# Optimization experiments

Hardware: AMD Instinct MI355X
Metric: run time of the kernel (lower is better)

## Reference

```python
import jax, jax.numpy as jnp
import numpy as np

N = 50000      # nodes
E = 400000     # edges
IN = 128       # in_channels
HID = 64       # hidden_channels (per head)
H = 4          # heads
OUT = 10       # classes
G = 64         # graphs in batch


def setup_inputs() -> dict:
    key = jax.random.key(0)
    ks = jax.random.split(key, 32)
    s = 0.05
    inp = {
        "x": jax.random.normal(ks[0], (N, IN), dtype=jnp.float32),
        "edge_index": jax.random.randint(ks[1], (2, E), 0, N, dtype=jnp.int32),
        "batch": jnp.sort(jax.random.randint(ks[2], (N,), 0, G, dtype=jnp.int32)),
    }
    # TransformerConv layer 1 params (in=IN -> heads*HID)
    d1 = H * HID
    inp["Wq1"] = jax.random.normal(ks[3], (IN, d1)) * s
    inp["bq1"] = jnp.zeros((d1,), jnp.float32)
    inp["Wk1"] = jax.random.normal(ks[4], (IN, d1)) * s
    inp["bk1"] = jnp.zeros((d1,), jnp.float32)
    inp["Wv1"] = jax.random.normal(ks[5], (IN, d1)) * s
    inp["bv1"] = jnp.zeros((d1,), jnp.float32)
    inp["Ws1"] = jax.random.normal(ks[6], (IN, d1)) * s   # root/skip weight
    inp["bs1"] = jnp.zeros((d1,), jnp.float32)
    # TransformerConv layer 2 params (in=H*HID -> heads*HID)
    inp["Wq2"] = jax.random.normal(ks[7], (d1, d1)) * s
    inp["bq2"] = jnp.zeros((d1,), jnp.float32)
    inp["Wk2"] = jax.random.normal(ks[8], (d1, d1)) * s
    inp["bk2"] = jnp.zeros((d1,), jnp.float32)
    inp["Wv2"] = jax.random.normal(ks[9], (d1, d1)) * s
    inp["bv2"] = jnp.zeros((d1,), jnp.float32)
    inp["Ws2"] = jax.random.normal(ks[10], (d1, d1)) * s
    inp["bs2"] = jnp.zeros((d1,), jnp.float32)
    # final classifier
    inp["Wl"] = jax.random.normal(ks[11], (d1, OUT)) * s
    inp["bl"] = jnp.zeros((OUT,), jnp.float32)
    return inp


def transformer_conv(x, src, dst, Wq, bq, Wk, bk, Wv, bv, Ws, bs):
    """PyG TransformerConv (concat=True, root_weight=True, beta=None, eval mode).
    src = edge_index[0] (source j), dst = edge_index[1] (target i).
    """
    n = x.shape[0]
    q = (x @ Wq + bq).reshape(n, H, HID)
    k = (x @ Wk + bk).reshape(n, H, HID)
    v = (x @ Wv + bv).reshape(n, H, HID)
    # per-edge attention logits [E, H]
    alpha = jnp.einsum('ehc,ehc->eh', q[dst], k[src]) / np.sqrt(HID).astype(np.float32)
    # scatter-softmax over incoming edges of each target node
    amax = jax.ops.segment_max(alpha, dst, num_segments=n)           # [N, H], -inf for isolated
    ex = jnp.exp(alpha - amax[dst])                                   # [E, H]
    denom = jax.ops.segment_sum(ex, dst, num_segments=n) + 1e-16      # [N, H]
    w = ex / denom[dst]                                               # normalized alpha [E, H]
    # scatter-sum aggregation of weighted values
    out = jax.ops.segment_sum(w[:, :, None] * v[src], dst, num_segments=n)  # [N, H, HID]
    out = out.reshape(n, H * HID)
    return out + (x @ Ws + bs)  # root/skip connection


def reference(x, edge_index, batch,
              Wq1, bq1, Wk1, bk1, Wv1, bv1, Ws1, bs1,
              Wq2, bq2, Wk2, bk2, Wv2, bv2, Ws2, bs2,
              Wl, bl):
    src, dst = edge_index[0], edge_index[1]
    h = jax.nn.elu(transformer_conv(x, src, dst, Wq1, bq1, Wk1, bk1, Wv1, bv1, Ws1, bs1))
    h = jax.nn.elu(transformer_conv(h, src, dst, Wq2, bq2, Wk2, bk2, Wv2, bv2, Ws2, bs2))
    # global mean pool per graph
    sums = jax.ops.segment_sum(h, batch, num_segments=G)              # [G, H*HID]
    cnt = jax.ops.segment_sum(jnp.ones((h.shape[0],), h.dtype), batch, num_segments=G)
    pooled = sums / jnp.maximum(cnt, 1.0)[:, None]
    logits = pooled @ Wl + bl
    return jax.nn.log_softmax(logits, axis=-1)
```

## Files before the change

kernel.cpp:

```cpp
#include <hip/hip_runtime.h>
#include <math.h>

constexpr int NN   = 50000;
constexpr int NE   = 400000;
constexpr int INC  = 128;
constexpr int NH   = 4;
constexpr int D1   = 256;
constexpr int D4   = 1024;
constexpr int NOUT = 10;
constexpr int NG   = 64;
constexpr int NB_SCAN = (NN + 255) / 256;


typedef __attribute__((ext_vector_type(8))) short bf16x8;
typedef __attribute__((ext_vector_type(4))) float f32x4;
typedef __attribute__((ext_vector_type(2))) float f32x2;

__device__ __forceinline__ short f2b(float f) {
  union { float f; unsigned int i; } v; v.f = f;
  unsigned int x = v.i;
  return (short)((x + 0x7FFFu + ((x >> 16) & 1u)) >> 16);
}
__device__ __forceinline__ float b2f(short u) {
  union { unsigned int i; float f; } v; v.i = ((unsigned int)(unsigned short)u) << 16;
  return v.f;
}
__device__ __forceinline__ float4 ld4b(const short* p) {
  short4 u = *(const short4*)p;
  return make_float4(b2f(u.x), b2f(u.y), b2f(u.z), b2f(u.w));
}
__device__ __forceinline__ void unpack8(const int4 v, float* f) {
  union { unsigned int u; float x; } a;
  a.u = (unsigned int)v.x << 16;         f[0] = a.x;
  a.u = (unsigned int)v.x & 0xffff0000u; f[1] = a.x;
  a.u = (unsigned int)v.y << 16;         f[2] = a.x;
  a.u = (unsigned int)v.y & 0xffff0000u; f[3] = a.x;
  a.u = (unsigned int)v.z << 16;         f[4] = a.x;
  a.u = (unsigned int)v.z & 0xffff0000u; f[5] = a.x;
  a.u = (unsigned int)v.w << 16;         f[6] = a.x;
  a.u = (unsigned int)v.w & 0xffff0000u; f[7] = a.x;
}
__device__ __forceinline__ int pk_fp8x4(float a, float b, float c, float d) {
  int v = __builtin_amdgcn_cvt_pk_fp8_f32(a, b, 0, false);
  v = __builtin_amdgcn_cvt_pk_fp8_f32(c, d, v, true);
  return v;
}

__device__ __forceinline__ void gld_lds16(const short* g, short* l) {
  __builtin_amdgcn_global_load_lds(
      (const __attribute__((address_space(1))) unsigned int*)g,
      (__attribute__((address_space(3))) unsigned int*)l, 16, 0, 0);
}

constexpr int CVT_XB  = (NN * INC / 4 + 255) / 256;
constexpr int CVT_W1B = (4 * D1 * INC + 255) / 256;
constexpr int CVT_W2B = (4 * D1 * D1 + 255) / 256;
constexpr int CVT_BB  = 8;
constexpr int CVT_DB  = (NN + 255) / 256;
constexpr int CVT_SB  = (NG * D1 + 255) / 256;

__device__ __forceinline__ void wt_one(const float* Wq, const float* Wk,
    const float* Wv, const float* Ws, short* Wt, int kbits, int i) {
  int K = 1 << kbits;
  int seg = i >> (kbits + 8);
  int idx = i & ((D1 << kbits) - 1);
  int n = idx >> kbits, k = idx & (K - 1);
  const float* W = (seg == 0) ? Wq : (seg == 1) ? Wk : (seg == 2) ? Wv : Ws;
  int row;
  if (seg == 0)      row = n;
  else if (seg == 3) row = 768 + n;
  else               row = 256 + (n >> 2) * 8 + ((seg == 2) ? 4 : 0) + (n & 3);
  Wt[(size_t)row * K + k] = f2b(W[(size_t)k * D1 + n]);
}

__global__ void cvt_all_k(const float* __restrict__ x, short* __restrict__ Xb,
    const float* __restrict__ Wq1, const float* __restrict__ Wk1,
    const float* __restrict__ Wv1, const float* __restrict__ Ws1,
    const float* __restrict__ Wq2, const float* __restrict__ Wk2,
    const float* __restrict__ Wv2, const float* __restrict__ Ws2,
    short* __restrict__ Wtc1, short* __restrict__ Wtc2,
    const float* __restrict__ bq1, const float* __restrict__ bk1,
    const float* __restrict__ bv1, const float* __restrict__ bs1,
    const float* __restrict__ bq2, const float* __restrict__ bk2,
    const float* __restrict__ bv2, const float* __restrict__ bs2,
    float* __restrict__ bc1, float* __restrict__ bc2,
    int* __restrict__ deg, float* __restrict__ sums) {
  const int b = blockIdx.x;
  const int t = threadIdx.x;
  if (b < CVT_XB) {
    int i = (b * 256 + t) * 4;
    if (i >= NN * INC) return;
    float4 v = *(const float4*)(x + i);
    short4 o; o.x = f2b(v.x); o.y = f2b(v.y); o.z = f2b(v.z); o.w = f2b(v.w);
    *(short4*)(Xb + i) = o;
  } else if (b < CVT_XB + CVT_W1B) {
    int i = (b - CVT_XB) * 256 + t;
    if (i < 4 * D1 * INC) wt_one(Wq1, Wk1, Wv1, Ws1, Wtc1, 7, i);
  } else if (b < CVT_XB + CVT_W1B + CVT_W2B) {
    int i = (b - CVT_XB - CVT_W1B) * 256 + t;
    if (i < 4 * D1 * D1) wt_one(Wq2, Wk2, Wv2, Ws2, Wtc2, 8, i);
  } else if (b < CVT_XB + CVT_W1B + CVT_W2B + CVT_BB) {
    int i = (b - CVT_XB - CVT_W1B - CVT_W2B) * 256 + t;
    if (i >= 2 * D4) return;
    int row = i & (D4 - 1);
    const float* bq = (i < D4) ? bq1 : bq2;
    const float* bk = (i < D4) ? bk1 : bk2;
    const float* bv = (i < D4) ? bv1 : bv2;
    const float* bs = (i < D4) ? bs1 : bs2;
    float v;
    if (row < 256) v = bq[row];
    else if (row < 768) {
      int j = row - 256, grp = j >> 3, off = j & 7;
      int ch = grp * 4 + (off & 3);
      v = (off < 4) ? bk[ch] : bv[ch];
    } else v = bs[row - 768];
    ((i < D4) ? bc1 : bc2)[row] = v;
  } else if (b < CVT_XB + CVT_W1B + CVT_W2B + CVT_BB + CVT_DB) {
    int i = (b - CVT_XB - CVT_W1B - CVT_W2B - CVT_BB) * 256 + t;
    if (i < NN) deg[i] = 0;
  } else {
    int i = (b - CVT_XB - CVT_W1B - CVT_W2B - CVT_BB - CVT_DB) * 256 + t;
    if (i < NG * D1) sums[i] = 0.f;
  }
}

__global__ void deg_count(const int* __restrict__ dst, int* __restrict__ deg) {
  int e = blockIdx.x * 256 + threadIdx.x;
  if (e < NE) atomicAdd(&deg[dst[e]], 1);
}
__global__ __launch_bounds__(256) void scan1(const int* __restrict__ deg,
    int* __restrict__ partial, const int* __restrict__ batch, int* __restrict__ gb) {
  if (blockIdx.x == NB_SCAN) {
    int g = threadIdx.x;
    if (g > NG) return;
    int lo = 0, hi = NN;
    while (lo < hi) {
      int mid = (lo + hi) >> 1;
      if (batch[mid] < g) lo = mid + 1; else hi = mid;
    }
    gb[g] = lo;
    return;
  }
  __shared__ int sh[256];
  int t = threadIdx.x, i = blockIdx.x * 256 + t;
  sh[t] = (i < NN) ? deg[i] : 0;
  __syncthreads();
  for (int off = 128; off > 0; off >>= 1) {
    if (t < off) sh[t] += sh[t + off];
    __syncthreads();
  }
  if (t == 0) partial[blockIdx.x] = sh[0];
}
__global__ __launch_bounds__(256) void scan3(const int* __restrict__ deg,
    const int* __restrict__ partial, int* __restrict__ rowstart,
    int* __restrict__ cursor) {
  __shared__ int sh[256];
  __shared__ int base_s;
  const int t = threadIdx.x;
  int pv = (t < NB_SCAN) ? partial[t] : 0;
  sh[t] = pv;
  __syncthreads();
  for (int off = 1; off < 256; off <<= 1) {
    int o = (t >= off) ? sh[t - off] : 0;
    __syncthreads();
    sh[t] += o;
    __syncthreads();
  }
  if (t == 0) base_s = (blockIdx.x == 0) ? 0 : sh[blockIdx.x - 1];
  __syncthreads();
  const int base = base_s;
  __syncthreads();
  int i = blockIdx.x * 256 + t;
  int v = (i < NN) ? deg[i] : 0;
  sh[t] = v;
  __syncthreads();
  for (int off = 1; off < 256; off <<= 1) {
    int o = (t >= off) ? sh[t - off] : 0;
    __syncthreads();
    sh[t] += o;
    __syncthreads();
  }
  int excl = sh[t] - v + base;
  if (i <= NN) rowstart[i] = excl;
  if (i < NN)  cursor[i]   = excl;
}
__global__ void scatter_k(const int* __restrict__ src, const int* __restrict__ dst,
    int* __restrict__ cursor, int* __restrict__ esrc) {
  int e = blockIdx.x * 256 + threadIdx.x;
  if (e >= NE) return;
  int d = dst[e];
  int pos = atomicAdd(&cursor[d], 1);
  esrc[pos] = src[e];
}

constexpr int CLDS = 136;

__global__ __launch_bounds__(256) void gemm_mfma(
    const short* __restrict__ Xb, const short* __restrict__ Wt,
    const float* __restrict__ bias, short* __restrict__ QS,
    unsigned char* __restrict__ KV8, int M, int K) {
  __shared__ short smem[128 * CLDS];
  short* As0 = smem;
  short* As1 = smem + 4096;
  short* Bs0 = smem + 8192;
  short* Bs1 = smem + 12288;
  const int bx = blockIdx.x;
  const int by = blockIdx.y;
  const int m_tile = (bx & 7) + (by << 3);
  const int n_tile = bx >> 3;
  const int m0 = m_tile * 128;
  if (m0 >= M) return;
  const int n0 = n_tile * 128;

  const int t    = threadIdx.x;
  const int lane = t & 63;
  const int wv   = t >> 6;
  const int wm   = (wv >> 1) * 64;
  const int wn   = (wv & 1) * 64;
  const int quad = lane >> 4;
  const int l16  = lane & 15;
  const int lrow = lane >> 2;
  const int lseg = lane & 3;

  f32x4 acc[4][4] = {};
  for (int k0 = 0; k0 < K; k0 += 64) {
#pragma unroll
    for (int j = 0; j < 2; ++j) {
      const int rb = wv * 32 + j * 16;
      int gm = m0 + rb + lrow;
      gm = gm < M ? gm : M - 1;
      const size_t ga = (size_t)gm * K + k0 + lseg * 8;
      gld_lds16(Xb + ga,      &As0[rb * 32]);
      gld_lds16(Xb + ga + 32, &As1[rb * 32]);
      const size_t gw = (size_t)(n0 + rb + lrow) * K + k0 + lseg * 8;
      gld_lds16(Wt + gw,      &Bs0[rb * 32]);
      gld_lds16(Wt + gw + 32, &Bs1[rb * 32]);
    }
    __syncthreads();
    {
      bf16x8 a[4], b[4];
#pragma unroll
      for (int mi = 0; mi < 4; mi++)
        a[mi] = *(const bf16x8*)(&As0[(wm + mi * 16 + l16) * 32 + quad * 8]);
#pragma unroll
      for (int nj = 0; nj < 4; nj++)
        b[nj] = *(const bf16x8*)(&Bs0[(wn + nj * 16 + l16) * 32 + quad * 8]);
#pragma unroll
      for (int mi = 0; mi < 4; mi++)
#pragma unroll
        for (int nj = 0; nj < 4; nj++)
          acc[mi][nj] = __builtin_amdgcn_mfma_f32_16x16x32_bf16(a[mi], b[nj], acc[mi][nj], 0, 0, 0);
#pragma unroll
      for (int mi = 0; mi < 4; mi++)
        a[mi] = *(const bf16x8*)(&As1[(wm + mi * 16 + l16) * 32 + quad * 8]);
#pragma unroll
      for (int nj = 0; nj < 4; nj++)
        b[nj] = *(const bf16x8*)(&Bs1[(wn + nj * 16 + l16) * 32 + quad * 8]);
#pragma unroll
      for (int mi = 0; mi < 4; mi++)
#pragma unroll
        for (int nj = 0; nj < 4; nj++)
          acc[mi][nj] = __builtin_amdgcn_mfma_f32_16x16x32_bf16(a[mi], b[nj], acc[mi][nj], 0, 0, 0);
    }
    __syncthreads();
  }
  float bcol[4];
#pragma unroll
  for (int nj = 0; nj < 4; nj++) bcol[nj] = bias[n0 + wn + nj * 16 + l16];
#pragma unroll
  for (int mi = 0; mi < 4; mi++)
#pragma unroll
    for (int r = 0; r < 4; r++) {
      const int row = wm + mi * 16 + quad * 4 + r;
#pragma unroll
      for (int nj = 0; nj < 4; nj++)
        smem[row * CLDS + wn + nj * 16 + l16] = f2b(acc[mi][nj][r] + bcol[nj]);
    }
  __syncthreads();
  const bool isKV = (n_tile >= 2) && (n_tile <= 5);
  const int qs_base = (n_tile < 2) ? n0 : (n0 - 512);
  const int kv_base = n0 - 256;
#pragma unroll
  for (int it = 0; it < 8; ++it) {
    const int chunk = it * 256 + t;
    const int row = chunk >> 4;
    const int cc  = (chunk & 15) * 8;
    const int gm  = m0 + row;
    if (gm >= M) continue;
    const int4 s4 = *(const int4*)(&smem[row * CLDS + cc]);
    if (isKV) {
      float f[8];
      unpack8(s4, f);
      int lo = pk_fp8x4(f[0], f[1], f[2], f[3]);
      int hi = pk_fp8x4(f[4], f[5], f[6], f[7]);
      *(int2*)(KV8 + (size_t)gm * 512 + kv_base + cc) = make_int2(lo, hi);
    } else {
      *(int4*)(QS + (size_t)gm * 512 + qs_base + cc) = s4;
    }
  }
}

__device__ __forceinline__ void dec_kv(const int2 x, float* k, float* v) {
  f32x2 a = __builtin_amdgcn_cvt_pk_f32_fp8(x.x, false);
  f32x2 b = __builtin_amdgcn_cvt_pk_f32_fp8(x.x, true);
  f32x2 c = __builtin_amdgcn_cvt_pk_f32_fp8(x.y, false);
  f32x2 d = __builtin_amdgcn_cvt_pk_f32_fp8(x.y, true);
  k[0] = a.x; k[1] = a.y; k[2] = b.x; k[3] = b.y;
  v[0] = c.x; v[1] = c.y; v[2] = d.x; v[3] = d.y;
}

template <typename TOUT>
__device__ __forceinline__ void st1(TOUT* p, float v);
template <> __device__ __forceinline__ void st1<float>(float* p, float v) { *p = v; }
template <> __device__ __forceinline__ void st1<short>(short* p, float v) { *p = f2b(v); }

template <typename TOUT>
__global__ __launch_bounds__(256) void node_attn(
    const int* __restrict__ rowstart, const int* __restrict__ esrc,
    const short* __restrict__ QS, const unsigned char* __restrict__ KV8,
    TOUT* __restrict__ out) {
  const int nid = blockIdx.x * 4 + (threadIdx.x >> 6);
  if (nid >= NN) return;
  const int t  = threadIdx.x & 63;
  const int c0 = t * 4;
  const int r0 = rowstart[nid], r1 = rowstart[nid + 1];
  const float4 q = ld4b(QS + (size_t)nid * 512 + c0);
  const unsigned char* kvb = KV8 + t * 8;
  float m = -INFINITY, denom = 0.f;
  float4 acc = make_float4(0.f, 0.f, 0.f, 0.f);
  int r = r0;
  for (; r + 3 < r1; r += 4) {
    const int2 x0 = *(const int2*)(kvb + (size_t)esrc[r + 0] * 512);
    const int2 x1 = *(const int2*)(kvb + (size_t)esrc[r + 1] * 512);
    const int2 x2 = *(const int2*)(kvb + (size_t)esrc[r + 2] * 512);
    const int2 x3 = *(const int2*)(kvb + (size_t)esrc[r + 3] * 512);
    float k0[4], v0[4], k1[4], v1[4], k2[4], v2[4], k3[4], v3[4];
    dec_kv(x0, k0, v0); dec_kv(x1, k1, v1);
    dec_kv(x2, k2, v2); dec_kv(x3, k3, v3);
    float d0 = q.x * k0[0] + q.y * k0[1] + q.z * k0[2] + q.w * k0[3];
    float d1 = q.x * k1[0] + q.y * k1[1] + q.z * k1[2] + q.w * k1[3];
    float d2 = q.x * k2[0] + q.y * k2[1] + q.z * k2[2] + q.w * k2[3];
    float d3 = q.x * k3[0] + q.y * k3[1] + q.z * k3[2] + q.w * k3[3];
#pragma unroll
    for (int off = 1; off <= 8; off <<= 1) {
      d0 += __shfl_xor(d0, off, 16);
      d1 += __shfl_xor(d1, off, 16);
      d2 += __shfl_xor(d2, off, 16);
      d3 += __shfl_xor(d3, off, 16);
    }
    d0 *= 0.125f; d1 *= 0.125f; d2 *= 0.125f; d3 *= 0.125f;
    const float nm = fmaxf(fmaxf(m, fmaxf(d0, d1)), fmaxf(d2, d3));
    const float sc = __expf(m - nm);
    const float e0 = __expf(d0 - nm);
    const float e1 = __expf(d1 - nm);
    const float e2 = __expf(d2 - nm);
    const float e3 = __expf(d3 - nm);
    denom = denom * sc + e0 + e1 + e2 + e3;
    acc.x = acc.x * sc + e0 * v0[0] + e1 * v1[0] + e2 * v2[0] + e3 * v3[0];
    acc.y = acc.y * sc + e0 * v0[1] + e1 * v1[1] + e2 * v2[1] + e3 * v3[1];
    acc.z = acc.z * sc + e0 * v0[2] + e1 * v1[2] + e2 * v2[2] + e3 * v3[2];
    acc.w = acc.w * sc + e0 * v0[3] + e1 * v1[3] + e2 * v2[3] + e3 * v3[3];
    m = nm;
  }
  for (; r < r1; r++) {
    const int2 x0 = *(const int2*)(kvb + (size_t)esrc[r] * 512);
    float k0[4], v0[4];
    dec_kv(x0, k0, v0);
    float d0 = q.x * k0[0] + q.y * k0[1] + q.z * k0[2] + q.w * k0[3];
#pragma unroll
    for (int off = 1; off <= 8; off <<= 1) d0 += __shfl_xor(d0, off, 16);
    d0 *= 0.125f;
    const float nm = fmaxf(m, d0);
    const float sc = __expf(m - nm);
    const float e0 = __expf(d0 - nm);
    denom = denom * sc + e0;
    acc.x = acc.x * sc + e0 * v0[0];
    acc.y = acc.y * sc + e0 * v0[1];
    acc.z = acc.z * sc + e0 * v0[2];
    acc.w = acc.w * sc + e0 * v0[3];
    m = nm;
  }
  const float inv = 1.0f / (denom + 1e-16f);
  const float4 sk = ld4b(QS + (size_t)nid * 512 + 256 + c0);
  float o0 = acc.x * inv + sk.x;
  float o1 = acc.y * inv + sk.y;
  float o2 = acc.z * inv + sk.z;
  float o3 = acc.w * inv + sk.w;
  o0 = o0 > 0.f ? o0 : expm1f(o0);
  o1 = o1 > 0.f ? o1 : expm1f(o1);
  o2 = o2 > 0.f ? o2 : expm1f(o2);
  o3 = o3 > 0.f ? o3 : expm1f(o3);
  TOUT* p = out + (size_t)nid * D1 + c0;
  st1<TOUT>(p + 0, o0); st1<TOUT>(p + 1, o1);
  st1<TOUT>(p + 2, o2); st1<TOUT>(p + 3, o3);
}

__global__ __launch_bounds__(256) void pool_k(const float* __restrict__ h,
    const int* __restrict__ batch, float* __restrict__ sums) {
  const int c = threadIdx.x;
  const int n0 = blockIdx.x * 64;
  const int n1 = min(n0 + 64, NN);
  float run = 0.f;
  int curg = -1;
  for (int n = n0; n < n1; n++) {
    int g = batch[n];
    if (g != curg) {
      if (curg >= 0) atomicAdd(&sums[(size_t)curg * D1 + c], run);
      run = 0.f; curg = g;
    }
    run += h[(size_t)n * D1 + c];
  }
  if (curg >= 0) atomicAdd(&sums[(size_t)curg * D1 + c], run);
}

__global__ __launch_bounds__(640) void head_k(const float* __restrict__ sums,
    const int* __restrict__ gb, const float* __restrict__ Wl,
    const float* __restrict__ bl, float* __restrict__ out) {
  __shared__ float logits[NG][NOUT];
  const int t = threadIdx.x;
  if (t < NG * NOUT) {
    int g = t / NOUT, o = t % NOUT;
    float inv = 1.0f / fmaxf((float)(gb[g + 1] - gb[g]), 1.0f);
    float acc = 0.f;
    for (int k = 0; k < D1; k++) acc += sums[(size_t)g * D1 + k] * Wl[k * NOUT + o];
    logits[g][o] = acc * inv + bl[o];
  }
  __syncthreads();
  if (t < NG) {
    float mx = -INFINITY;
#pragma unroll
    for (int o = 0; o < NOUT; o++) mx = fmaxf(mx, logits[t][o]);
    float s = 0.f;
#pragma unroll
    for (int o = 0; o < NOUT; o++) s += __expf(logits[t][o] - mx);
    float lse = mx + logf(s);
#pragma unroll
    for (int o = 0; o < NOUT; o++) out[t * NOUT + o] = logits[t][o] - lse;
  }
}

extern "C" void kernel_launch(void* const* d_in, const int* in_sizes, int n_in,
                              void* d_out, int out_size, void* d_ws, size_t ws_size,
                              hipStream_t stream) {
  const float* x   = (const float*)d_in[0];
  const int* ei    = (const int*)d_in[1];
  const int* batch = (const int*)d_in[2];
  const float* Wq1 = (const float*)d_in[3];  const float* bq1 = (const float*)d_in[4];
  const float* Wk1 = (const float*)d_in[5];  const float* bk1 = (const float*)d_in[6];
  const float* Wv1 = (const float*)d_in[7];  const float* bv1 = (const float*)d_in[8];
  const float* Ws1 = (const float*)d_in[9];  const float* bs1 = (const float*)d_in[10];
  const float* Wq2 = (const float*)d_in[11]; const float* bq2 = (const float*)d_in[12];
  const float* Wk2 = (const float*)d_in[13]; const float* bk2 = (const float*)d_in[14];
  const float* Wv2 = (const float*)d_in[15]; const float* bv2 = (const float*)d_in[16];
  const float* Ws2 = (const float*)d_in[17]; const float* bs2 = (const float*)d_in[18];
  const float* Wl  = (const float*)d_in[19]; const float* bl  = (const float*)d_in[20];

  const int* srcIdx = ei;
  const int* dstIdx = ei + NE;

  float* ws = (float*)d_ws;
  const size_t SZ_NODE = (size_t)NN * D1;
  float* H2f  = ws;
  float* sums = ws + SZ_NODE;
  float* bc1  = sums + (size_t)NG * D1;
  float* bc2  = bc1 + D4;
  short* Xb   = (short*)(bc2 + D4);
  short* H1b  = Xb + (size_t)NN * INC;
  short* QS   = H1b + SZ_NODE;
  short* Wtc1 = QS + (size_t)NN * 512;
  short* Wtc2 = Wtc1 + (size_t)D4 * INC;
  unsigned char* KV8 = (unsigned char*)(Wtc2 + (size_t)D4 * D1);
  int* ip      = (int*)(KV8 + (size_t)NN * 512);
  int* deg     = ip;
  int* partial = deg + NN;
  int* rowstart= partial + 256;
  int* cursor  = rowstart + NN + 1;
  int* esrc    = cursor + NN;
  int* gb      = esrc + NE;

  const int mtiles = (NN + 127) / 128;
  const dim3 gemmGrid(64, (mtiles + 7) / 8);
  const int edgeBlocks = (NE + 255) / 256;
  const int aggBlocks  = (NN + 3) / 4;
  const int cvtBlocks  = CVT_XB + CVT_W1B + CVT_W2B + CVT_BB + CVT_DB + CVT_SB;

  cvt_all_k<<<cvtBlocks, 256, 0, stream>>>(x, Xb,
      Wq1, Wk1, Wv1, Ws1, Wq2, Wk2, Wv2, Ws2, Wtc1, Wtc2,
      bq1, bk1, bv1, bs1, bq2, bk2, bv2, bs2, bc1, bc2, deg, sums);

  deg_count<<<edgeBlocks, 256, 0, stream>>>(dstIdx, deg);
  scan1<<<NB_SCAN + 1, 256, 0, stream>>>(deg, partial, batch, gb);
  scan3<<<NB_SCAN, 256, 0, stream>>>(deg, partial, rowstart, cursor);
  scatter_k<<<edgeBlocks, 256, 0, stream>>>(srcIdx, dstIdx, cursor, esrc);

  gemm_mfma<<<gemmGrid, 256, 0, stream>>>(Xb, Wtc1, bc1, QS, KV8, NN, INC);
  node_attn<short><<<aggBlocks, 256, 0, stream>>>(rowstart, esrc, QS, KV8, H1b);

  gemm_mfma<<<gemmGrid, 256, 0, stream>>>(H1b, Wtc2, bc2, QS, KV8, NN, D1);
  node_attn<float><<<aggBlocks, 256, 0, stream>>>(rowstart, esrc, QS, KV8, H2f);

  pool_k<<<(NN + 63) / 64, 256, 0, stream>>>(H2f, batch, sums);
  head_k<<<1, 640, 0, stream>>>(sums, gb, Wl, bl, (float*)d_out);
}
```

Baseline: 367.7 us.

## Swizzle GEMM LDS, store epilogue from registers, unroll node attention by eight

New measurement: 398.1 us. 8.3% more time.

```diff
diff --git a/kernel.cpp b/kernel.cpp
--- a/kernel.cpp
+++ b/kernel.cpp
@@ -28,17 +28,6 @@
 __device__ __forceinline__ float4 ld4b(const short* p) {
   short4 u = *(const short4*)p;
   return make_float4(b2f(u.x), b2f(u.y), b2f(u.z), b2f(u.w));
-}
-__device__ __forceinline__ void unpack8(const int4 v, float* f) {
-  union { unsigned int u; float x; } a;
-  a.u = (unsigned int)v.x << 16;         f[0] = a.x;
-  a.u = (unsigned int)v.x & 0xffff0000u; f[1] = a.x;
-  a.u = (unsigned int)v.y << 16;         f[2] = a.x;
-  a.u = (unsigned int)v.y & 0xffff0000u; f[3] = a.x;
-  a.u = (unsigned int)v.z << 16;         f[4] = a.x;
-  a.u = (unsigned int)v.z & 0xffff0000u; f[5] = a.x;
-  a.u = (unsigned int)v.w << 16;         f[6] = a.x;
-  a.u = (unsigned int)v.w & 0xffff0000u; f[7] = a.x;
 }
 __device__ __forceinline__ int pk_fp8x4(float a, float b, float c, float d) {
   int v = __builtin_amdgcn_cvt_pk_fp8_f32(a, b, 0, false);
@@ -193,13 +182,11 @@
   esrc[pos] = src[e];
 }
 
-constexpr int CLDS = 136;
-
 __global__ __launch_bounds__(256) void gemm_mfma(
     const short* __restrict__ Xb, const short* __restrict__ Wt,
     const float* __restrict__ bias, short* __restrict__ QS,
     unsigned char* __restrict__ KV8, int M, int K) {
-  __shared__ short smem[128 * CLDS];
+  __shared__ short smem[4 * 4096];
   short* As0 = smem;
   short* As1 = smem + 4096;
   short* Bs0 = smem + 8192;
@@ -222,6 +209,9 @@
   const int lrow = lane >> 2;
   const int lseg = lane & 3;
 
+  const int swz_w = (lseg ^ ((lrow >> 1) & 3)) * 8;
+  const int swz_r = (quad ^ ((l16 >> 1) & 3)) * 8;
+
   f32x4 acc[4][4] = {};
   for (int k0 = 0; k0 < K; k0 += 64) {
 #pragma unroll
@@ -229,10 +219,10 @@
       const int rb = wv * 32 + j * 16;
       int gm = m0 + rb + lrow;
       gm = gm < M ? gm : M - 1;
-      const size_t ga = (size_t)gm * K + k0 + lseg * 8;
+      const size_t ga = (size_t)gm * K + k0 + swz_w;
       gld_lds16(Xb + ga,      &As0[rb * 32]);
       gld_lds16(Xb + ga + 32, &As1[rb * 32]);
-      const size_t gw = (size_t)(n0 + rb + lrow) * K + k0 + lseg * 8;
+      const size_t gw = (size_t)(n0 + rb + lrow) * K + k0 + swz_w;
       gld_lds16(Wt + gw,      &Bs0[rb * 32]);
       gld_lds16(Wt + gw + 32, &Bs1[rb * 32]);
     }
@@ -241,61 +231,54 @@
       bf16x8 a[4], b[4];
 #pragma unroll
       for (int mi = 0; mi < 4; mi++)
-        a[mi] = *(const bf16x8*)(&As0[(wm + mi * 16 + l16) * 32 + quad * 8]);
+        a[mi] = *(const bf16x8*)(&As0[(wm + mi * 16 + l16) * 32 + swz_r]);
 #pragma unroll
       for (int nj = 0; nj < 4; nj++)
-        b[nj] = *(const bf16x8*)(&Bs0[(wn + nj * 16 + l16) * 32 + quad * 8]);
+        b[nj] = *(const bf16x8*)(&Bs0[(wn + nj * 16 + l16) * 32 + swz_r]);
 #pragma unroll
       for (int mi = 0; mi < 4; mi++)
 #pragma unroll
         for (int nj = 0; nj < 4; nj++)
-          acc[mi][nj] = __builtin_amdgcn_mfma_f32_16x16x32_bf16(a[mi], b[nj], acc[mi][nj], 0, 0, 0);
+          acc[mi][nj] = __builtin_amdgcn_mfma_f32_16x16x32_bf16(b[nj], a[mi], acc[mi][nj], 0, 0, 0);
 #pragma unroll
       for (int mi = 0; mi < 4; mi++)
-        a[mi] = *(const bf16x8*)(&As1[(wm + mi * 16 + l16) * 32 + quad * 8]);
+        a[mi] = *(const bf16x8*)(&As1[(wm + mi * 16 + l16) * 32 + swz_r]);
 #pragma unroll
       for (int nj = 0; nj < 4; nj++)
-        b[nj] = *(const bf16x8*)(&Bs1[(wn + nj * 16 + l16) * 32 + quad * 8]);
+        b[nj] = *(const bf16x8*)(&Bs1[(wn + nj * 16 + l16) * 32 + swz_r]);
 #pragma unroll
       for (int mi = 0; mi < 4; mi++)
 #pragma unroll
         for (int nj = 0; nj < 4; nj++)
-          acc[mi][nj] = __builtin_amdgcn_mfma_f32_16x16x32_bf16(a[mi], b[nj], acc[mi][nj], 0, 0, 0);
-    }
-    __syncthreads();
-  }
-  float bcol[4];
-#pragma unroll
-  for (int nj = 0; nj < 4; nj++) bcol[nj] = bias[n0 + wn + nj * 16 + l16];
-#pragma unroll
-  for (int mi = 0; mi < 4; mi++)
-#pragma unroll
-    for (int r = 0; r < 4; r++) {
-      const int row = wm + mi * 16 + quad * 4 + r;
-#pragma unroll
-      for (int nj = 0; nj < 4; nj++)
-        smem[row * CLDS + wn + nj * 16 + l16] = f2b(acc[mi][nj][r] + bcol[nj]);
-    }
-  __syncthreads();
+          acc[mi][nj] = __builtin_amdgcn_mfma_f32_16x16x32_bf16(b[nj], a[mi], acc[mi][nj], 0, 0, 0);
+    }
+    __syncthreads();
+  }
   const bool isKV = (n_tile >= 2) && (n_tile <= 5);
-  const int qs_base = (n_tile < 2) ? n0 : (n0 - 512);
-  const int kv_base = n0 - 256;
-#pragma unroll
-  for (int it = 0; it < 8; ++it) {
-    const int chunk = it * 256 + t;
-    const int row = chunk >> 4;
-    const int cc  = (chunk & 15) * 8;
-    const int gm  = m0 + row;
-    if (gm >= M) continue;
-    const int4 s4 = *(const int4*)(&smem[row * CLDS + cc]);
-    if (isKV) {
-      float f[8];
-      unpack8(s4, f);
-      int lo = pk_fp8x4(f[0], f[1], f[2], f[3]);
-      int hi = pk_fp8x4(f[4], f[5], f[6], f[7]);
-      *(int2*)(KV8 + (size_t)gm * 512 + kv_base + cc) = make_int2(lo, hi);
-    } else {
-      *(int4*)(QS + (size_t)gm * 512 + qs_base + cc) = s4;
+  float4 bz[4];
+#pragma unroll
+  for (int nj = 0; nj < 4; nj++)
+    bz[nj] = *(const float4*)(bias + n0 + wn + nj * 16 + quad * 4);
+#pragma unroll
+  for (int mi = 0; mi < 4; mi++) {
+    const int m = m0 + wm + mi * 16 + l16;
+    if (m >= M) continue;
+#pragma unroll
+    for (int nj = 0; nj < 4; nj++) {
+      const int col = n0 + wn + nj * 16 + quad * 4;
+      const float v0 = acc[mi][nj][0] + bz[nj].x;
+      const float v1 = acc[mi][nj][1] + bz[nj].y;
+      const float v2 = acc[mi][nj][2] + bz[nj].z;
+      const float v3 = acc[mi][nj][3] + bz[nj].w;
+      if (isKV) {
+        const int p = pk_fp8x4(v0, v1, v2, v3);
+        *(int*)(KV8 + (size_t)m * 512 + (col - 256)) = p;
+      } else {
+        short4 o;
+        o.x = f2b(v0); o.y = f2b(v1); o.z = f2b(v2); o.w = f2b(v3);
+        const int qc = (n_tile < 2) ? col : (col - 512);
+        *(short4*)(QS + (size_t)m * 512 + qc) = o;
+      }
     }
   }
 }
@@ -323,17 +306,89 @@
   if (nid >= NN) return;
   const int t  = threadIdx.x & 63;
   const int c0 = t * 4;
-  const int r0 = rowstart[nid], r1 = rowstart[nid + 1];
+  const int r0 = __builtin_amdgcn_readfirstlane(rowstart[nid]);
+  const int r1 = __builtin_amdgcn_readfirstlane(rowstart[nid + 1]);
   const float4 q = ld4b(QS + (size_t)nid * 512 + c0);
   const unsigned char* kvb = KV8 + t * 8;
   float m = -INFINITY, denom = 0.f;
   float4 acc = make_float4(0.f, 0.f, 0.f, 0.f);
   int r = r0;
+  for (; r + 7 < r1; r += 8) {
+    const int e0 = __builtin_amdgcn_readfirstlane(esrc[r + 0]);
+    const int e1 = __builtin_amdgcn_readfirstlane(esrc[r + 1]);
+    const int e2 = __builtin_amdgcn_readfirstlane(esrc[r + 2]);
+    const int e3 = __builtin_amdgcn_readfirstlane(esrc[r + 3]);
+    const int e4 = __builtin_amdgcn_readfirstlane(esrc[r + 4]);
+    const int e5 = __builtin_amdgcn_readfirstlane(esrc[r + 5]);
+    const int e6 = __builtin_amdgcn_readfirstlane(esrc[r + 6]);
+    const int e7 = __builtin_amdgcn_readfirstlane(esrc[r + 7]);
+    const int2 x0 = *(const int2*)(kvb + (size_t)e0 * 512);
+    const int2 x1 = *(const int2*)(kvb + (size_t)e1 * 512);
+    const int2 x2 = *(const int2*)(kvb + (size_t)e2 * 512);
+    const int2 x3 = *(const int2*)(kvb + (size_t)e3 * 512);
+    const int2 x4 = *(const int2*)(kvb + (size_t)e4 * 512);
+    const int2 x5 = *(const int2*)(kvb + (size_t)e5 * 512);
+    const int2 x6 = *(const int2*)(kvb + (size_t)e6 * 512);
+    const int2 x7 = *(const int2*)(kvb + (size_t)e7 * 512);
+    float k0[4], v0[4], k1[4], v1[4], k2[4], v2[4], k3[4], v3[4];
+    float k4[4], v4[4], k5[4], v5[4], k6[4], v6[4], k7[4], v7[4];
+    dec_kv(x0, k0, v0); dec_kv(x1, k1, v1);
+    dec_kv(x2, k2, v2); dec_kv(x3, k3, v3);
+    dec_kv(x4, k4, v4); dec_kv(x5, k5, v5);
+    dec_kv(x6, k6, v6); dec_kv(x7, k7, v7);
+    float d0 = q.x * k0[0] + q.y * k0[1] + q.z * k0[2] + q.w * k0[3];
+    float d1 = q.x * k1[0] + q.y * k1[1] + q.z * k1[2] + q.w * k1[3];
+    float d2 = q.x * k2[0] + q.y * k2[1] + q.z * k2[2] + q.w * k2[3];
+    float d3 = q.x * k3[0] + q.y * k3[1] + q.z * k3[2] + q.w * k3[3];
+    float d4 = q.x * k4[0] + q.y * k4[1] + q.z * k4[2] + q.w * k4[3];
+    float d5 = q.x * k5[0] + q.y * k5[1] + q.z * k5[2] + q.w * k5[3];
+    float d6 = q.x * k6[0] + q.y * k6[1] + q.z * k6[2] + q.w * k6[3];
+    float d7 = q.x * k7[0] + q.y * k7[1] + q.z * k7[2] + q.w * k7[3];
+#pragma unroll
+    for (int off = 1; off <= 8; off <<= 1) {
+      d0 += __shfl_xor(d0, off, 16);
+      d1 += __shfl_xor(d1, off, 16);
+      d2 += __shfl_xor(d2, off, 16);
+      d3 += __shfl_xor(d3, off, 16);
+      d4 += __shfl_xor(d4, off, 16);
+      d5 += __shfl_xor(d5, off, 16);
+      d6 += __shfl_xor(d6, off, 16);
+      d7 += __shfl_xor(d7, off, 16);
+    }
+    d0 *= 0.125f; d1 *= 0.125f; d2 *= 0.125f; d3 *= 0.125f;
+    d4 *= 0.125f; d5 *= 0.125f; d6 *= 0.125f; d7 *= 0.125f;
+    const float t01 = fmaxf(d0, d1), t23 = fmaxf(d2, d3);
+    const float t45 = fmaxf(d4, d5), t67 = fmaxf(d6, d7);
+    const float nm = fmaxf(fmaxf(m, fmaxf(t01, t23)), fmaxf(t45, t67));
+    const float sc  = __expf(m - nm);
+    const float ex0 = __expf(d0 - nm);
+    const float ex1 = __expf(d1 - nm);
+    const float ex2 = __expf(d2 - nm);
+    const float ex3 = __expf(d3 - nm);
+    const float ex4 = __expf(d4 - nm);
+    const float ex5 = __expf(d5 - nm);
+    const float ex6 = __expf(d6 - nm);
+    const float ex7 = __expf(d7 - nm);
+    denom = denom * sc + ((ex0 + ex1) + (ex2 + ex3)) + ((ex4 + ex5) + (ex6 + ex7));
+    acc.x = acc.x * sc + ex0 * v0[0] + ex1 * v1[0] + ex2 * v2[0] + ex3 * v3[0]
+                       + ex4 * v4[0] + ex5 * v5[0] + ex6 * v6[0] + ex7 * v7[0];
+    acc.y = acc.y * sc + ex0 * v0[1] + ex1 * v1[1] + ex2 * v2[1] + ex3 * v3[1]
+                       + ex4 * v4[1] + ex5 * v5[1] + ex6 * v6[1] + ex7 * v7[1];
+    acc.z = acc.z * sc + ex0 * v0[2] + ex1 * v1[2] + ex2 * v2[2] + ex3 * v3[2]
+                       + ex4 * v4[2] + ex5 * v5[2] + ex6 * v6[2] + ex7 * v7[2];
+    acc.w = acc.w * sc + ex0 * v0[3] + ex1 * v1[3] + ex2 * v2[3] + ex3 * v3[3]
+                       + ex4 * v4[3] + ex5 * v5[3] + ex6 * v6[3] + ex7 * v7[3];
+    m = nm;
+  }
   for (; r + 3 < r1; r += 4) {
-    const int2 x0 = *(const int2*)(kvb + (size_t)esrc[r + 0] * 512);
-    const int2 x1 = *(const int2*)(kvb + (size_t)esrc[r + 1] * 512);
-    const int2 x2 = *(const int2*)(kvb + (size_t)esrc[r + 2] * 512);
-    const int2 x3 = *(const int2*)(kvb + (size_t)esrc[r + 3] * 512);
+    const int e0 = __builtin_amdgcn_readfirstlane(esrc[r + 0]);
+    const int e1 = __builtin_amdgcn_readfirstlane(esrc[r + 1]);
+    const int e2 = __builtin_amdgcn_readfirstlane(esrc[r + 2]);
+    const int e3 = __builtin_amdgcn_readfirstlane(esrc[r + 3]);
+    const int2 x0 = *(const int2*)(kvb + (size_t)e0 * 512);
+    const int2 x1 = *(const int2*)(kvb + (size_t)e1 * 512);
+    const int2 x2 = *(const int2*)(kvb + (size_t)e2 * 512);
+    const int2 x3 = *(const int2*)(kvb + (size_t)e3 * 512);
     float k0[4], v0[4], k1[4], v1[4], k2[4], v2[4], k3[4], v3[4];
     dec_kv(x0, k0, v0); dec_kv(x1, k1, v1);
     dec_kv(x2, k2, v2); dec_kv(x3, k3, v3);
@@ -351,19 +406,20 @@
     d0 *= 0.125f; d1 *= 0.125f; d2 *= 0.125f; d3 *= 0.125f;
     const float nm = fmaxf(fmaxf(m, fmaxf(d0, d1)), fmaxf(d2, d3));
     const float sc = __expf(m - nm);
-    const float e0 = __expf(d0 - nm);
-    const float e1 = __expf(d1 - nm);
-    const float e2 = __expf(d2 - nm);
-    const float e3 = __expf(d3 - nm);
-    denom = denom * sc + e0 + e1 + e2 + e3;
-    acc.x = acc.x * sc + e0 * v0[0] + e1 * v1[0] + e2 * v2[0] + e3 * v3[0];
-    acc.y = acc.y * sc + e0 * v0[1] + e1 * v1[1] + e2 * v2[1] + e3 * v3[1];
-    acc.z = acc.z * sc + e0 * v0[2] + e1 * v1[2] + e2 * v2[2] + e3 * v3[2];
-    acc.w = acc.w * sc + e0 * v0[3] + e1 * v1[3] + e2 * v2[3] + e3 * v3[3];
+    const float ex0 = __expf(d0 - nm);
+    const float ex1 = __expf(d1 - nm);
+    const float ex2 = __expf(d2 - nm);
+    const float ex3 = __expf(d3 - nm);
+    denom = denom * sc + ex0 + ex1 + ex2 + ex3;
+    acc.x = acc.x * sc + ex0 * v0[0] + ex1 * v1[0] + ex2 * v2[0] + ex3 * v3[0];
+    acc.y = acc.y * sc + ex0 * v0[1] + ex1 * v1[1] + ex2 * v2[1] + ex3 * v3[1];
+    acc.z = acc.z * sc + ex0 * v0[2] + ex1 * v1[2] + ex2 * v2[2] + ex3 * v3[2];
+    acc.w = acc.w * sc + ex0 * v0[3] + ex1 * v1[3] + ex2 * v2[3] + ex3 * v3[3];
     m = nm;
   }
   for (; r < r1; r++) {
-    const int2 x0 = *(const int2*)(kvb + (size_t)esrc[r] * 512);
+    const int e0 = __builtin_amdgcn_readfirstlane(esrc[r]);
+    const int2 x0 = *(const int2*)(kvb + (size_t)e0 * 512);
     float k0[4], v0[4];
     dec_kv(x0, k0, v0);
     float d0 = q.x * k0[0] + q.y * k0[1] + q.z * k0[2] + q.w * k0[3];
@@ -372,12 +428,12 @@
     d0 *= 0.125f;
     const float nm = fmaxf(m, d0);
     const float sc = __expf(m - nm);
-    const float e0 = __expf(d0 - nm);
-    denom = denom * sc + e0;
-    acc.x = acc.x * sc + e0 * v0[0];
-    acc.y = acc.y * sc + e0 * v0[1];
-    acc.z = acc.z * sc + e0 * v0[2];
-    acc.w = acc.w * sc + e0 * v0[3];
+    const float ex0 = __expf(d0 - nm);
+    denom = denom * sc + ex0;
+    acc.x = acc.x * sc + ex0 * v0[0];
+    acc.y = acc.y * sc + ex0 * v0[1];
+    acc.z = acc.z * sc + ex0 * v0[2];
+    acc.w = acc.w * sc + ex0 * v0[3];
     m = nm;
   }
   const float inv = 1.0f / (denom + 1e-16f);
```
